# Kernel optimization log

Hardware: AMD Instinct MI355X
Metric: run time of the kernel (lower is better)

## Reference

```python
import jax, jax.numpy as jnp
import numpy as np

HEAD_NUM = 16

def setup_inputs() -> dict:
    key = jax.random.key(0)
    kx, kid, kw1, kw2 = jax.random.split(key, 4)
    bs, seq_len, dim = 4, 2048, 2048
    x = jax.random.normal(kx, (bs, seq_len, dim), dtype=jnp.float32)
    ids = jnp.sort(jax.random.randint(kid, (bs, seq_len), 0, 8), axis=-1).astype(jnp.int32)
    Wqkv = jax.random.normal(kw1, (dim, 3 * dim), dtype=jnp.float32) * 0.02
    bqkv = jnp.zeros((3 * dim,), dtype=jnp.float32)
    Wo = jax.random.normal(kw2, (dim, dim), dtype=jnp.float32) * 0.02
    bo = jnp.zeros((dim,), dtype=jnp.float32)
    return {"x": x, "ids": ids, "Wqkv": Wqkv, "bqkv": bqkv, "Wo": Wo, "bo": bo}

def reference(x, ids, Wqkv, bqkv, Wo, bo):
    bs, seq_len, dim = x.shape
    H = HEAD_NUM
    hd = dim // H
    qkv = x @ Wqkv + bqkv                      # [bs, S, 3*dim]
    q, k, v = jnp.split(qkv, 3, axis=-1)
    q = q.reshape(bs, seq_len, H, hd).transpose(0, 2, 1, 3)  # [bs,H,S,hd]
    k = k.reshape(bs, seq_len, H, hd).transpose(0, 2, 1, 3)
    v = v.reshape(bs, seq_len, H, hd).transpose(0, 2, 1, 3)
    q = q / jnp.asarray(hd, q.dtype) ** 0.5
    score = jnp.einsum('bhqd,bhkd->bhqk', q, k)              # [bs,H,S,S]
    # segment mask: block attention across different segment ids
    seg_mask = ids[:, None, :, None] != ids[:, None, None, :]  # [bs,1,S,S]
    # causal mask: block j > i
    causal_mask = jnp.triu(jnp.ones((seq_len, seq_len), dtype=bool), k=1)[None, None]
    mask = seg_mask | causal_mask
    score = jnp.where(mask, -jnp.inf, score)
    score = score - jnp.max(score, axis=-1, keepdims=True)
    attn = jax.nn.softmax(score, axis=-1)
    out = jnp.einsum('bhqk,bhkd->bhqd', attn, v)             # [bs,H,S,hd]
    out = out.transpose(0, 2, 1, 3).reshape(bs, seq_len, dim)
    return out @ Wo + bo
```

## Files before the change

kernel.cpp:

```cpp
#include <hip/hip_runtime.h>
#include <hip/hip_bf16.h>
#include <stdint.h>

#define DEVFN static __device__ __forceinline__

typedef __attribute__((ext_vector_type(8))) __bf16 bf16x8;
typedef __attribute__((ext_vector_type(4))) float floatx4;

DEVFN uint16_t f2bf(float f) {
    uint32_t u = __builtin_bit_cast(uint32_t, f);
    uint32_t r = u + 0x7fffu + ((u >> 16) & 1u);
    return (uint16_t)(r >> 16);
}

DEVFN void gload_lds16(const void* g, void* l) {
    __builtin_amdgcn_global_load_lds(
        (__attribute__((address_space(1))) void*)(g),
        (__attribute__((address_space(3))) void*)(l), 16, 0, 0);
}

#define BAR() asm volatile("s_barrier" ::: "memory")
#define VM4() asm volatile("s_waitcnt vmcnt(4)" ::: "memory")

__global__ void mha_cast_vec(const float* __restrict__ in, uint16_t* __restrict__ out, int n) {
    const int stride = gridDim.x * blockDim.x * 4;
    for (int i = (blockIdx.x * blockDim.x + threadIdx.x) * 4; i < n; i += stride) {
        const float4 v = *reinterpret_cast<const float4*>(in + i);
        ushort4 o = make_ushort4(f2bf(v.x), f2bf(v.y), f2bf(v.z), f2bf(v.w));
        *reinterpret_cast<ushort4*>(out + i) = o;
    }
}

__global__ void mha_transpose_cast(const float* __restrict__ in, uint16_t* __restrict__ out,
                                   int R, int C) {
    __shared__ uint16_t t[32][33];
    const int c0 = blockIdx.x * 32, r0 = blockIdx.y * 32;
    for (int dr = threadIdx.y; dr < 32; dr += 8)
        t[dr][threadIdx.x] = f2bf(in[(size_t)(r0 + dr) * C + c0 + threadIdx.x]);
    __syncthreads();
    for (int dc = threadIdx.y; dc < 32; dc += 8)
        out[(size_t)(c0 + dc) * R + r0 + threadIdx.x] = t[threadIdx.x][dc];
}


#define STG(P, HALF, C, LB)                                                              \
    do {                                                                                 \
        gload_lds16((P) + (size_t)((HALF) * 128) * K + (C), lds + (LB) + w * 1024);      \
        gload_lds16((P) + (size_t)((HALF) * 128 + 64) * K + (C),                         \
                    lds + (LB) + 8192 + w * 1024);                                       \
    } while (0)

#define LDA(BUF, MB)                                                                     \
    do {                                                                                 \
        _Pragma("unroll") for (int m_ = 0; m_ < 4; ++m_)                                 \
        _Pragma("unroll") for (int k_ = 0; k_ < 2; ++k_) {                               \
            const int rih_ = ((MB) + m_) * 16 + l16;                                     \
            af[m_][k_] = *(const bf16x8*)(lds + (BUF) * 65536 + wm * 16384 + rih_ * 128  \
                                          + ((k_ * 64 + lhi * 16) ^ ((rih_ & 7) << 4))); \
        }                                                                                \
    } while (0)

#define LDB(DST, BUF, NB)                                                                \
    do {                                                                                 \
        _Pragma("unroll") for (int n_ = 0; n_ < 2; ++n_)                                 \
        _Pragma("unroll") for (int k_ = 0; k_ < 2; ++k_) {                               \
            const int row_ = wn * 64 + ((NB) + n_) * 16 + l16;                           \
            DST[n_][k_] = *(const bf16x8*)(lds + (BUF) * 65536 + 32768                   \
                                           + (row_ >> 7) * 16384 + (row_ & 127) * 128    \
                                           + ((k_ * 64 + lhi * 16) ^ ((row_ & 7) << 4))); \
        }                                                                                \
    } while (0)

#define QUAD(MB, NB, BF)                                                                 \
    do {                                                                                 \
        __builtin_amdgcn_s_setprio(1);                                                   \
        _Pragma("unroll") for (int k_ = 0; k_ < 2; ++k_)                                 \
        _Pragma("unroll") for (int m_ = 0; m_ < 4; ++m_)                                 \
        _Pragma("unroll") for (int n_ = 0; n_ < 2; ++n_)                                 \
            acc[(MB) + m_][(NB) + n_] = __builtin_amdgcn_mfma_f32_16x16x32_bf16(         \
                af[m_][k_], BF[n_][k_], acc[(MB) + m_][(NB) + n_], 0, 0, 0);             \
        __builtin_amdgcn_s_setprio(0);                                                   \
    } while (0)

template <int MODE>
__global__ __launch_bounds__(512, 2) void mha_gemm8(
    const uint16_t* __restrict__ A, const uint16_t* __restrict__ Bt,
    const float* __restrict__ bias,
    uint16_t* __restrict__ oQ, uint16_t* __restrict__ oK, uint16_t* __restrict__ oVt,
    float* __restrict__ oF,
    int M, int N, int K) {
    extern __shared__ char lds[];
    const int tid = threadIdx.x, lane = tid & 63, w = tid >> 6;
    const int wm = w >> 2, wn = w & 3;
    const int l16 = lane & 15, lhi = lane >> 4;
    const int xcd = blockIdx.x & 7;
    const int idx = blockIdx.x >> 3;
    const int c4 = idx >> 4, rem = idx & 15;
    const int m0 = (xcd * 4 + (rem >> 2)) * 256;
    const int n0 = (c4 * 4 + (rem & 3)) * 256;

    const int NKT = K >> 6;
    const int NI = K >> 7;

    floatx4 acc[8][4] = {};
    bf16x8 af[4][2], bl[2][2], bh[2][2];

    const int rbase = w * 8 + (lane >> 3);
    const int slot8 = ((lane & 7) ^ (rbase & 7)) * 8;
    const uint16_t* pA0 = A + (size_t)(m0 + rbase) * K + slot8;
    const uint16_t* pB0 = Bt + (size_t)(n0 + rbase) * K + slot8;

    STG(pA0, 0, 0, 0);
    STG(pA0, 1, 0, 16384);
    STG(pB0, 0, 0, 32768);
    STG(pB0, 1, 0, 49152);
    STG(pB0, 0, 64, 65536 + 32768);
    STG(pB0, 1, 64, 65536 + 49152);
    VM4();
    BAR();

    for (int i = 0; i < NI; ++i) {
        const int c1 = (2 * i + 1) * 64;
        const int c2 = (2 * i + 2 < NKT ? 2 * i + 2 : 0) * 64;
        const int c3 = (2 * i + 3 < NKT ? 2 * i + 3 : 0) * 64;
        LDA(0, 0);
        LDB(bl, 0, 0);
        STG(pA0, 0, c1, 65536);
        BAR();
        QUAD(0, 0, bl);
        BAR();
        LDB(bh, 0, 2);
        STG(pA0, 1, c1, 65536 + 16384);
        BAR();
        QUAD(0, 2, bh);
        BAR();
        LDA(0, 4);
        STG(pB0, 0, c2, 32768);
        BAR();
        QUAD(4, 0, bl);
        BAR();
        STG(pB0, 1, c2, 49152);
        VM4();
        BAR();
        QUAD(4, 2, bh);
        BAR();
        LDA(1, 0);
        LDB(bl, 1, 0);
        STG(pA0, 0, c2, 0);
        BAR();
        QUAD(0, 0, bl);
        BAR();
        LDB(bh, 1, 2);
        STG(pA0, 1, c2, 16384);
        BAR();
        QUAD(0, 2, bh);
        BAR();
        LDA(1, 4);
        STG(pB0, 0, c3, 65536 + 32768);
        BAR();
        QUAD(4, 0, bl);
        BAR();
        STG(pB0, 1, c3, 65536 + 49152);
        VM4();
        BAR();
        QUAD(4, 2, bh);
        BAR();
    }

#pragma unroll
    for (int mf = 0; mf < 8; ++mf) {
        const int mb = m0 + wm * 128 + mf * 16 + lhi * 4;
#pragma unroll
        for (int nf = 0; nf < 4; ++nf) {
            const int n = n0 + wn * 64 + nf * 16 + l16;
            const float bb = bias[n];
            if (MODE == 0) {
                const int which = n >> 11, h = (n >> 7) & 15, d = n & 127;
                const int b = mb >> 11, s = mb & 2047;
                if (which == 2) {
                    ushort4 vv;
                    vv.x = f2bf(acc[mf][nf][0] + bb);
                    vv.y = f2bf(acc[mf][nf][1] + bb);
                    vv.z = f2bf(acc[mf][nf][2] + bb);
                    vv.w = f2bf(acc[mf][nf][3] + bb);
                    *(ushort4*)(oVt + ((size_t)(b * 16 + h) * 128 + d) * 2048 + s) = vv;
                } else {
                    uint16_t* dst = (which == 0) ? oQ : oK;
                    const float sc = (which == 0) ? 0.08838834764831845f : 1.0f;
#pragma unroll
                    for (int r = 0; r < 4; ++r)
                        dst[((size_t)(b * 16 + h) * 2048 + (s + r)) * 128 + d] =
                            f2bf((acc[mf][nf][r] + bb) * sc);
                }
            } else {
#pragma unroll
                for (int r = 0; r < 4; ++r)
                    oF[(size_t)(mb + r) * N + n] = acc[mf][nf][r] + bb;
            }
        }
    }
}

__global__ __launch_bounds__(256) void mha_attn(
    const uint16_t* __restrict__ Qg, const uint16_t* __restrict__ Kg,
    const uint16_t* __restrict__ Vtg, const int* __restrict__ ids,
    uint16_t* __restrict__ Ao) {
    constexpr int S = 2048, HD = 128;
    __shared__ __align__(16) uint16_t Ks[64 * 128];
    __shared__ __align__(16) uint16_t Vs[128 * 64];
    __shared__ __align__(16) uint16_t Ps[4][16 * 64];

    const int tid = threadIdx.x, lane = tid & 63, w = tid >> 6;
    const int l16 = lane & 15, lhi = lane >> 4;
    const int qt = blockIdx.x, bh = blockIdx.y;
    const int b = bh >> 4, h = bh & 15;
    const size_t base = (size_t)bh * S * HD;
    const int q0 = qt * 64, qw0 = q0 + w * 16;
    const int* idb = ids + b * S;

    bf16x8 qf[4];
#pragma unroll
    for (int c = 0; c < 4; ++c)
        qf[c] = *(const bf16x8*)&Qg[base + (size_t)(qw0 + l16) * HD + c * 32 + lhi * 8];

    int idq[4];
#pragma unroll
    for (int r = 0; r < 4; ++r) idq[r] = idb[qw0 + lhi * 4 + r];
    const int qid_min = idb[q0];

    floatx4 o[8] = {};
    float lrow[4] = {0.f, 0.f, 0.f, 0.f};

    const int krow = lane >> 4, kcol = (lane & 15) * 16;
    const int vrow = lane >> 3, vcol = (lane & 7) * 16;

    for (int kt = 0; kt <= qt; ++kt) {
        const int k0 = kt * 64;
        if (idb[k0 + 63] < qid_min) continue;
        __syncthreads();
#pragma unroll
        for (int c = 0; c < 4; ++c) {
            const int cc = w * 4 + c;
            const int rr = cc * 4 + krow;
            gload_lds16((const char*)Kg + (base + (size_t)(k0 + rr) * HD) * 2 +
                            (kcol ^ ((rr & 7) << 4)),
                        (char*)Ks + cc * 1024);
            const int vr = cc * 8 + vrow;
            gload_lds16((const char*)Vtg + (base + (size_t)vr * S + k0) * 2 +
                            (vcol ^ ((vr & 7) << 4)),
                        (char*)Vs + cc * 1024);
        }
        __syncthreads();

        floatx4 sa[4] = {};
#pragma unroll
        for (int fc = 0; fc < 4; ++fc)
#pragma unroll
            for (int c = 0; c < 4; ++c) {
                bf16x8 kf = *(const bf16x8*)((const char*)Ks + (fc * 16 + l16) * 256 +
                                             ((c * 64 + lhi * 16) ^ ((l16 & 7) << 4)));
                sa[fc] = __builtin_amdgcn_mfma_f32_16x16x32_bf16(qf[c], kf, sa[fc], 0, 0, 0);
            }

        int idk[4];
#pragma unroll
        for (int fc = 0; fc < 4; ++fc) idk[fc] = idb[k0 + fc * 16 + l16];

#pragma unroll
        for (int r = 0; r < 4; ++r) {
            const int q = qw0 + lhi * 4 + r;
            const int prow = lhi * 4 + r;
            float rs = 0.f;
#pragma unroll
            for (int fc = 0; fc < 4; ++fc) {
                const int k = k0 + fc * 16 + l16;
                const bool valid = (k <= q) && (idk[fc] == idq[r]);
                const float pv = valid ? __expf(sa[fc][r]) : 0.f;
                *(uint16_t*)((char*)Ps + w * 2048 + prow * 128 +
                             (((fc * 16 + l16) * 2) ^ ((prow & 7) << 4))) = f2bf(pv);
                rs += pv;
            }
            lrow[r] += rs;
        }

#pragma unroll
        for (int kk = 0; kk < 2; ++kk) {
            bf16x8 pa = *(const bf16x8*)((const char*)Ps + w * 2048 + l16 * 128 +
                                         ((kk * 64 + lhi * 16) ^ ((l16 & 7) << 4)));
#pragma unroll
            for (int f2 = 0; f2 < 8; ++f2) {
                bf16x8 vf = *(const bf16x8*)((const char*)Vs + (f2 * 16 + l16) * 128 +
                                             ((kk * 64 + lhi * 16) ^ ((l16 & 7) << 4)));
                o[f2] = __builtin_amdgcn_mfma_f32_16x16x32_bf16(pa, vf, o[f2], 0, 0, 0);
            }
        }
    }

#pragma unroll
    for (int r = 0; r < 4; ++r) {
        float ls = lrow[r];
        ls += __shfl_xor(ls, 1);
        ls += __shfl_xor(ls, 2);
        ls += __shfl_xor(ls, 4);
        ls += __shfl_xor(ls, 8);
        const float inv = 1.0f / ls;
        const int q = qw0 + lhi * 4 + r;
        uint16_t* dst = Ao + ((size_t)(b * 2048) + q) * 2048 + h * 128;
#pragma unroll
        for (int f2 = 0; f2 < 8; ++f2)
            dst[f2 * 16 + l16] = f2bf(o[f2][r] * inv);
    }
}

extern "C" void kernel_launch(void* const* d_in, const int* in_sizes, int n_in,
                              void* d_out, int out_size, void* d_ws, size_t ws_size,
                              hipStream_t stream) {
    const float* x = (const float*)d_in[0];
    const int* ids = (const int*)d_in[1];
    const float* Wqkv = (const float*)d_in[2];
    const float* bqkv = (const float*)d_in[3];
    const float* Wo = (const float*)d_in[4];
    const float* bo = (const float*)d_in[5];
    float* out = (float*)d_out;

    uint16_t* ws = (uint16_t*)d_ws;
    uint16_t* xb = ws;
    uint16_t* WqkvT = xb + 16777216;
    uint16_t* WoT = WqkvT + 12582912;
    uint16_t* Qb = WoT + 4194304;
    uint16_t* Kb = Qb + 16777216;
    uint16_t* Vtb = Kb + 16777216;
    uint16_t* Ao = xb;

    hipFuncSetAttribute((const void*)&mha_gemm8<0>,
                        hipFuncAttributeMaxDynamicSharedMemorySize, 131072);
    hipFuncSetAttribute((const void*)&mha_gemm8<1>,
                        hipFuncAttributeMaxDynamicSharedMemorySize, 131072);

    mha_cast_vec<<<2048, 256, 0, stream>>>(x, xb, 16777216);
    mha_transpose_cast<<<dim3(192, 64), dim3(32, 8), 0, stream>>>(Wqkv, WqkvT, 2048, 6144);
    mha_transpose_cast<<<dim3(64, 64), dim3(32, 8), 0, stream>>>(Wo, WoT, 2048, 2048);

    mha_gemm8<0><<<768, 512, 131072, stream>>>(xb, WqkvT, bqkv, Qb, Kb, Vtb, nullptr,
                                               8192, 6144, 2048);
    mha_attn<<<dim3(32, 64), 256, 0, stream>>>(Qb, Kb, Vtb, ids, Ao);
    mha_gemm8<1><<<256, 512, 131072, stream>>>(Ao, WoT, bo, nullptr, nullptr, nullptr, out,
                                               8192, 2048, 2048);
}
```

Baseline: 480.9 us.

## Double attention query tile per block to reuse K/V tiles across two row groups

The attention kernel now handles 128 query rows per block instead of 64. Each wavefront processes two 16-row groups against the same K/V tile in LDS, which halves the global-to-LDS traffic and barriers per query row. Query blocks are launched in an interleaved order that mixes heavy and light causal rows, and launch bounds request 3 blocks per CU. In exchange, registers per thread roughly double, and the coarser tile skips fewer segment and causal tiles near the diagonal.

Result: slower. 516.9 us (+7.5%).

```diff
diff --git a/kernel.cpp b/kernel.cpp
--- a/kernel.cpp
+++ b/kernel.cpp
@@ -201,7 +201,7 @@
     }
 }
 
-__global__ __launch_bounds__(256) void mha_attn(
+__global__ __launch_bounds__(256, 3) void mha_attn(
     const uint16_t* __restrict__ Qg, const uint16_t* __restrict__ Kg,
     const uint16_t* __restrict__ Vtg, const int* __restrict__ ids,
     uint16_t* __restrict__ Ao) {
@@ -212,29 +212,36 @@
 
     const int tid = threadIdx.x, lane = tid & 63, w = tid >> 6;
     const int l16 = lane & 15, lhi = lane >> 4;
-    const int qt = blockIdx.x, bh = blockIdx.y;
+    const int bx = blockIdx.x, bh = blockIdx.y;
+    const int qb = (bx & 7) * 2 + (bx >> 3);
     const int b = bh >> 4, h = bh & 15;
     const size_t base = (size_t)bh * S * HD;
-    const int q0 = qt * 64, qw0 = q0 + w * 16;
+    const int q0 = qb * 128, qw0 = q0 + w * 32;
     const int* idb = ids + b * S;
 
-    bf16x8 qf[4];
-#pragma unroll
-    for (int c = 0; c < 4; ++c)
-        qf[c] = *(const bf16x8*)&Qg[base + (size_t)(qw0 + l16) * HD + c * 32 + lhi * 8];
-
-    int idq[4];
-#pragma unroll
-    for (int r = 0; r < 4; ++r) idq[r] = idb[qw0 + lhi * 4 + r];
+    bf16x8 qf[2][4];
+#pragma unroll
+    for (int mi = 0; mi < 2; ++mi)
+#pragma unroll
+        for (int c = 0; c < 4; ++c)
+            qf[mi][c] = *(const bf16x8*)&Qg[base + (size_t)(qw0 + mi * 16 + l16) * HD +
+                                            c * 32 + lhi * 8];
+
+    int idq[2][4];
+#pragma unroll
+    for (int mi = 0; mi < 2; ++mi)
+#pragma unroll
+        for (int r = 0; r < 4; ++r) idq[mi][r] = idb[qw0 + mi * 16 + lhi * 4 + r];
     const int qid_min = idb[q0];
 
-    floatx4 o[8] = {};
-    float lrow[4] = {0.f, 0.f, 0.f, 0.f};
+    floatx4 o[2][8] = {};
+    float lrow[2][4] = {};
 
     const int krow = lane >> 4, kcol = (lane & 15) * 16;
     const int vrow = lane >> 3, vcol = (lane & 7) * 16;
-
-    for (int kt = 0; kt <= qt; ++kt) {
+    const int ktmax = 2 * qb + 1;
+
+    for (int kt = 0; kt <= ktmax; ++kt) {
         const int k0 = kt * 64;
         if (idb[k0 + 63] < qid_min) continue;
         __syncthreads();
@@ -252,64 +259,71 @@
         }
         __syncthreads();
 
-        floatx4 sa[4] = {};
-#pragma unroll
-        for (int fc = 0; fc < 4; ++fc)
-#pragma unroll
-            for (int c = 0; c < 4; ++c) {
-                bf16x8 kf = *(const bf16x8*)((const char*)Ks + (fc * 16 + l16) * 256 +
-                                             ((c * 64 + lhi * 16) ^ ((l16 & 7) << 4)));
-                sa[fc] = __builtin_amdgcn_mfma_f32_16x16x32_bf16(qf[c], kf, sa[fc], 0, 0, 0);
+        int idk[4];
+#pragma unroll
+        for (int fc = 0; fc < 4; ++fc) idk[fc] = idb[k0 + fc * 16 + l16];
+
+#pragma unroll
+        for (int mi = 0; mi < 2; ++mi) {
+            floatx4 sa[4] = {};
+#pragma unroll
+            for (int fc = 0; fc < 4; ++fc)
+#pragma unroll
+                for (int c = 0; c < 4; ++c) {
+                    bf16x8 kf = *(const bf16x8*)((const char*)Ks + (fc * 16 + l16) * 256 +
+                                                 ((c * 64 + lhi * 16) ^ ((l16 & 7) << 4)));
+                    sa[fc] = __builtin_amdgcn_mfma_f32_16x16x32_bf16(qf[mi][c], kf, sa[fc],
+                                                                     0, 0, 0);
+                }
+
+#pragma unroll
+            for (int r = 0; r < 4; ++r) {
+                const int q = qw0 + mi * 16 + lhi * 4 + r;
+                const int prow = lhi * 4 + r;
+                float rs = 0.f;
+#pragma unroll
+                for (int fc = 0; fc < 4; ++fc) {
+                    const int k = k0 + fc * 16 + l16;
+                    const bool valid = (k <= q) && (idk[fc] == idq[mi][r]);
+                    const float pv = valid ? __expf(sa[fc][r]) : 0.f;
+                    *(uint16_t*)((char*)Ps + w * 2048 + prow * 128 +
+                                 (((fc * 16 + l16) * 2) ^ ((prow & 7) << 4))) = f2bf(pv);
+                    rs += pv;
+                }
+                lrow[mi][r] += rs;
             }
 
-        int idk[4];
-#pragma unroll
-        for (int fc = 0; fc < 4; ++fc) idk[fc] = idb[k0 + fc * 16 + l16];
-
-#pragma unroll
-        for (int r = 0; r < 4; ++r) {
-            const int q = qw0 + lhi * 4 + r;
-            const int prow = lhi * 4 + r;
-            float rs = 0.f;
-#pragma unroll
-            for (int fc = 0; fc < 4; ++fc) {
-                const int k = k0 + fc * 16 + l16;
-                const bool valid = (k <= q) && (idk[fc] == idq[r]);
-                const float pv = valid ? __expf(sa[fc][r]) : 0.f;
-                *(uint16_t*)((char*)Ps + w * 2048 + prow * 128 +
-                             (((fc * 16 + l16) * 2) ^ ((prow & 7) << 4))) = f2bf(pv);
-                rs += pv;
-            }
-            lrow[r] += rs;
-        }
-
-#pragma unroll
-        for (int kk = 0; kk < 2; ++kk) {
-            bf16x8 pa = *(const bf16x8*)((const char*)Ps + w * 2048 + l16 * 128 +
-                                         ((kk * 64 + lhi * 16) ^ ((l16 & 7) << 4)));
-#pragma unroll
-            for (int f2 = 0; f2 < 8; ++f2) {
-                bf16x8 vf = *(const bf16x8*)((const char*)Vs + (f2 * 16 + l16) * 128 +
+#pragma unroll
+            for (int kk = 0; kk < 2; ++kk) {
+                bf16x8 pa = *(const bf16x8*)((const char*)Ps + w * 2048 + l16 * 128 +
                                              ((kk * 64 + lhi * 16) ^ ((l16 & 7) << 4)));
-                o[f2] = __builtin_amdgcn_mfma_f32_16x16x32_bf16(pa, vf, o[f2], 0, 0, 0);
+#pragma unroll
+                for (int f2 = 0; f2 < 8; ++f2) {
+                    bf16x8 vf = *(const bf16x8*)((const char*)Vs + (f2 * 16 + l16) * 128 +
+                                                 ((kk * 64 + lhi * 16) ^ ((l16 & 7) << 4)));
+                    o[mi][f2] = __builtin_amdgcn_mfma_f32_16x16x32_bf16(pa, vf, o[mi][f2],
+                                                                        0, 0, 0);
+                }
             }
         }
     }
 
 #pragma unroll
-    for (int r = 0; r < 4; ++r) {
-        float ls = lrow[r];
-        ls += __shfl_xor(ls, 1);
-        ls += __shfl_xor(ls, 2);
-        ls += __shfl_xor(ls, 4);
-        ls += __shfl_xor(ls, 8);
-        const float inv = 1.0f / ls;
-        const int q = qw0 + lhi * 4 + r;
-        uint16_t* dst = Ao + ((size_t)(b * 2048) + q) * 2048 + h * 128;
-#pragma unroll
-        for (int f2 = 0; f2 < 8; ++f2)
-            dst[f2 * 16 + l16] = f2bf(o[f2][r] * inv);
-    }
+    for (int mi = 0; mi < 2; ++mi)
+#pragma unroll
+        for (int r = 0; r < 4; ++r) {
+            float ls = lrow[mi][r];
+            ls += __shfl_xor(ls, 1);
+            ls += __shfl_xor(ls, 2);
+            ls += __shfl_xor(ls, 4);
+            ls += __shfl_xor(ls, 8);
+            const float inv = 1.0f / ls;
+            const int q = qw0 + mi * 16 + lhi * 4 + r;
+            uint16_t* dst = Ao + ((size_t)(b * 2048) + q) * 2048 + h * 128;
+#pragma unroll
+            for (int f2 = 0; f2 < 8; ++f2)
+                dst[f2 * 16 + l16] = f2bf(o[mi][f2][r] * inv);
+        }
 }
 
 extern "C" void kernel_launch(void* const* d_in, const int* in_sizes, int n_in,
@@ -343,7 +357,7 @@
 
     mha_gemm8<0><<<768, 512, 131072, stream>>>(xb, WqkvT, bqkv, Qb, Kb, Vtb, nullptr,
                                                8192, 6144, 2048);
-    mha_attn<<<dim3(32, 64), 256, 0, stream>>>(Qb, Kb, Vtb, ids, Ao);
+    mha_attn<<<dim3(16, 64), 256, 0, stream>>>(Qb, Kb, Vtb, ids, Ao);
     mha_gemm8<1><<<256, 512, 131072, stream>>>(Ao, WoT, bo, nullptr, nullptr, nullptr, out,
                                                8192, 2048, 2048);
 }
```

## Read K/V fragments directly from global memory and drop LDS staging in attention

Applied to the files above, without the earlier changes.

The attention kernel stops staging K and V tiles through shared memory and loads the MFMA operand fragments straight from global memory. This removes both per-tile barriers, so each wave runs independently. The kernel also computes the first relevant key tile once instead of testing every tile, and remaps the 1D grid so query tiles of one head are interleaved. A launch-bounds occupancy hint is added as well. The cost is that each of the four waves now re-reads the same K/V data from global memory or cache with uncoalesced 16-byte row accesses, instead of sharing one LDS copy.

New measurement: 571.6 us. 1.19x slower.

```diff
diff --git a/kernel.cpp b/kernel.cpp
--- a/kernel.cpp
+++ b/kernel.cpp
@@ -201,18 +201,17 @@
     }
 }
 
-__global__ __launch_bounds__(256) void mha_attn(
+__global__ __launch_bounds__(256, 3) void mha_attn(
     const uint16_t* __restrict__ Qg, const uint16_t* __restrict__ Kg,
     const uint16_t* __restrict__ Vtg, const int* __restrict__ ids,
     uint16_t* __restrict__ Ao) {
     constexpr int S = 2048, HD = 128;
-    __shared__ __align__(16) uint16_t Ks[64 * 128];
-    __shared__ __align__(16) uint16_t Vs[128 * 64];
     __shared__ __align__(16) uint16_t Ps[4][16 * 64];
 
     const int tid = threadIdx.x, lane = tid & 63, w = tid >> 6;
     const int l16 = lane & 15, lhi = lane >> 4;
-    const int qt = blockIdx.x, bh = blockIdx.y;
+    const int lin = blockIdx.x;
+    const int bh = lin >> 5, qt = (lin & 7) * 4 + ((lin >> 3) & 3);
     const int b = bh >> 4, h = bh & 15;
     const size_t base = (size_t)bh * S * HD;
     const int q0 = qt * 64, qw0 = q0 + w * 16;
@@ -228,37 +227,23 @@
     for (int r = 0; r < 4; ++r) idq[r] = idb[qw0 + lhi * 4 + r];
     const int qid_min = idb[q0];
 
+    int kt0 = qt;
+    while (kt0 > 0 && idb[kt0 * 64 - 1] >= qid_min) --kt0;
+
     floatx4 o[8] = {};
     float lrow[4] = {0.f, 0.f, 0.f, 0.f};
 
-    const int krow = lane >> 4, kcol = (lane & 15) * 16;
-    const int vrow = lane >> 3, vcol = (lane & 7) * 16;
-
-    for (int kt = 0; kt <= qt; ++kt) {
+    for (int kt = kt0; kt <= qt; ++kt) {
         const int k0 = kt * 64;
-        if (idb[k0 + 63] < qid_min) continue;
-        __syncthreads();
-#pragma unroll
-        for (int c = 0; c < 4; ++c) {
-            const int cc = w * 4 + c;
-            const int rr = cc * 4 + krow;
-            gload_lds16((const char*)Kg + (base + (size_t)(k0 + rr) * HD) * 2 +
-                            (kcol ^ ((rr & 7) << 4)),
-                        (char*)Ks + cc * 1024);
-            const int vr = cc * 8 + vrow;
-            gload_lds16((const char*)Vtg + (base + (size_t)vr * S + k0) * 2 +
-                            (vcol ^ ((vr & 7) << 4)),
-                        (char*)Vs + cc * 1024);
-        }
-        __syncthreads();
+        const uint16_t* Kt = Kg + base + (size_t)k0 * HD;
+        const uint16_t* Vt = Vtg + base + k0;
 
         floatx4 sa[4] = {};
 #pragma unroll
         for (int fc = 0; fc < 4; ++fc)
 #pragma unroll
             for (int c = 0; c < 4; ++c) {
-                bf16x8 kf = *(const bf16x8*)((const char*)Ks + (fc * 16 + l16) * 256 +
-                                             ((c * 64 + lhi * 16) ^ ((l16 & 7) << 4)));
+                bf16x8 kf = *(const bf16x8*)&Kt[(size_t)(fc * 16 + l16) * HD + c * 32 + lhi * 8];
                 sa[fc] = __builtin_amdgcn_mfma_f32_16x16x32_bf16(qf[c], kf, sa[fc], 0, 0, 0);
             }
 
@@ -289,8 +274,7 @@
                                          ((kk * 64 + lhi * 16) ^ ((l16 & 7) << 4)));
 #pragma unroll
             for (int f2 = 0; f2 < 8; ++f2) {
-                bf16x8 vf = *(const bf16x8*)((const char*)Vs + (f2 * 16 + l16) * 128 +
-                                             ((kk * 64 + lhi * 16) ^ ((l16 & 7) << 4)));
+                bf16x8 vf = *(const bf16x8*)&Vt[(size_t)(f2 * 16 + l16) * S + kk * 32 + lhi * 8];
                 o[f2] = __builtin_amdgcn_mfma_f32_16x16x32_bf16(pa, vf, o[f2], 0, 0, 0);
             }
         }
@@ -343,7 +327,7 @@
 
     mha_gemm8<0><<<768, 512, 131072, stream>>>(xb, WqkvT, bqkv, Qb, Kb, Vtb, nullptr,
                                                8192, 6144, 2048);
-    mha_attn<<<dim3(32, 64), 256, 0, stream>>>(Qb, Kb, Vtb, ids, Ao);
+    mha_attn<<<2048, 256, 0, stream>>>(Qb, Kb, Vtb, ids, Ao);
     mha_gemm8<1><<<256, 512, 131072, stream>>>(Ao, WoT, bo, nullptr, nullptr, nullptr, out,
                                                8192, 2048, 2048);
 }
```
